# Optimization experiments

Measured on AMD Instinct MI355X. Metric: run time of the kernel, lower is better.

Reference implementation:

```python
import jax, jax.numpy as jnp
import numpy as np

EPS = 1e-5

def setup_inputs() -> dict:
    key = jax.random.key(0)
    kx, kq, kp = jax.random.split(key, 3)
    B, T, d = 4, 4096, 512
    x = jax.random.normal(kx, (B, T, d), dtype=jnp.float32)
    mask = jnp.tril(jnp.ones((T, T), dtype=jnp.int32))  # causal 0/1 mask
    gamma = jnp.ones((d,), dtype=jnp.float32)
    beta = jnp.zeros((d,), dtype=jnp.float32)
    Wqkv = jax.random.normal(kq, (d, 3 * d), dtype=jnp.float32) / np.sqrt(d)
    Wproj = jax.random.normal(kp, (d, d), dtype=jnp.float32) / np.sqrt(d)
    return {"x": x, "mask": mask, "gamma": gamma, "beta": beta, "Wqkv": Wqkv, "Wproj": Wproj}

def reference(x, mask, gamma, beta, Wqkv, Wproj):
    B, T, C = x.shape
    # LayerNorm over last dim
    mu = jnp.mean(x, axis=-1, keepdims=True)
    var = jnp.mean(jnp.square(x - mu), axis=-1, keepdims=True)
    xn = (x - mu) * jax.lax.rsqrt(var + EPS) * gamma + beta
    # QKV projection (no bias)
    qkv = xn @ Wqkv  # [B,T,3C]
    q, k, v = jnp.split(qkv, 3, axis=-1)
    scale = 1.0 / np.sqrt(C)
    dist = jnp.einsum('btc,bsc->bts', q, k) * scale  # [B,T,T]
    dist = jnp.where(mask[:T, :T] == 0, -jnp.inf, dist)
    attn = jax.nn.softmax(dist, axis=-1)
    out = jnp.einsum('bts,bsc->btc', attn, v)
    return out @ Wproj
```

## Files before the change

kernel.cpp:

```cpp
#include <hip/hip_runtime.h>

typedef short bf16x8 __attribute__((ext_vector_type(8)));
typedef float f32x4 __attribute__((ext_vector_type(4)));

#define AS1 __attribute__((address_space(1)))
#define AS3 __attribute__((address_space(3)))

__device__ __forceinline__ void async16(const void* g, void* l) {
    __builtin_amdgcn_global_load_lds((AS1 unsigned*)(unsigned long long)g,
                                     (AS3 unsigned*)l, 16, 0, 0);
}

__device__ __forceinline__ unsigned short f2bf(float f) {
    unsigned u = __builtin_bit_cast(unsigned, f);
    u += 0x7fffu + ((u >> 16) & 1u);
    return (unsigned short)(u >> 16);
}
__device__ __forceinline__ float bf2f(unsigned short s) {
    unsigned u = ((unsigned)s) << 16;
    return __builtin_bit_cast(float, u);
}

__global__ __launch_bounds__(256) void ln_bf16_kernel(
    const float* __restrict__ x, const float* __restrict__ gamma,
    const float* __restrict__ beta, unsigned short* __restrict__ xn, int nrows)
{
    int row = blockIdx.x * 4 + (threadIdx.x >> 6);
    int lane = threadIdx.x & 63;
    if (row >= nrows) return;
    const float4* xr = (const float4*)(x + (size_t)row * 512);
    float4 a = xr[lane], b = xr[lane + 64];
    float s = a.x + a.y + a.z + a.w + b.x + b.y + b.z + b.w;
    #pragma unroll
    for (int m = 1; m < 64; m <<= 1) s += __shfl_xor(s, m);
    float mu = s * (1.0f / 512.0f);
    float dx[8] = {a.x - mu, a.y - mu, a.z - mu, a.w - mu,
                   b.x - mu, b.y - mu, b.z - mu, b.w - mu};
    float ss = 0.f;
    #pragma unroll
    for (int i = 0; i < 8; ++i) ss += dx[i] * dx[i];
    #pragma unroll
    for (int m = 1; m < 64; m <<= 1) ss += __shfl_xor(ss, m);
    float rstd = rsqrtf(ss * (1.0f / 512.0f) + 1e-5f);
    const float4* gp = (const float4*)gamma;
    const float4* bp = (const float4*)beta;
    float4 g0 = gp[lane], g1 = gp[lane + 64], b0 = bp[lane], b1 = bp[lane + 64];
    float y[8];
    y[0] = dx[0] * rstd * g0.x + b0.x; y[1] = dx[1] * rstd * g0.y + b0.y;
    y[2] = dx[2] * rstd * g0.z + b0.z; y[3] = dx[3] * rstd * g0.w + b0.w;
    y[4] = dx[4] * rstd * g1.x + b1.x; y[5] = dx[5] * rstd * g1.y + b1.y;
    y[6] = dx[6] * rstd * g1.z + b1.z; y[7] = dx[7] * rstd * g1.w + b1.w;
    ushort4* orow = (ushort4*)(xn + (size_t)row * 512);
    orow[lane]      = make_ushort4(f2bf(y[0]), f2bf(y[1]), f2bf(y[2]), f2bf(y[3]));
    orow[lane + 64] = make_ushort4(f2bf(y[4]), f2bf(y[5]), f2bf(y[6]), f2bf(y[7]));
}

__global__ __launch_bounds__(256) void transpose_w2(
    const float* __restrict__ wqkv, const float* __restrict__ wproj,
    unsigned short* __restrict__ wqkvT, unsigned short* __restrict__ wprojT)
{
    __shared__ float tile[64][65];
    const int R = 512;
    int by = blockIdx.y;
    const float* in;
    unsigned short* outT;
    int Cd, c0;
    if (by < 24) { in = wqkv;  outT = wqkvT;  Cd = 1536; c0 = by * 64; }
    else         { in = wproj; outT = wprojT; Cd = 512;  c0 = (by - 24) * 64; }
    int r0 = blockIdx.x * 64;
    int lr = threadIdx.x >> 6, lc = threadIdx.x & 63;
    #pragma unroll
    for (int i = 0; i < 16; ++i) {
        int r = i * 4 + lr;
        tile[r][lc] = in[(size_t)(r0 + r) * Cd + c0 + lc];
    }
    __syncthreads();
    #pragma unroll
    for (int i = 0; i < 16; ++i) {
        int r = i * 4 + lr;
        outT[(size_t)(c0 + r) * R + r0 + lc] = f2bf(tile[lc][r]);
    }
}

__global__ __launch_bounds__(256) void gemm_qkv(
    const unsigned short* __restrict__ A, const unsigned short* __restrict__ Bt,
    unsigned short* __restrict__ qkOut, unsigned short* __restrict__ vtp)
{
    __shared__ unsigned short As[128 * 64];
    __shared__ unsigned short Bs[128 * 64];
    const int tid = threadIdx.x;
    const int w = tid >> 6, lane = tid & 63, quad = lane >> 4, l15 = lane & 15;
    const int wm = w >> 1, wn = w & 1;
    const size_t m0 = (size_t)blockIdx.x * 128, n0 = (size_t)blockIdx.y * 128;
    f32x4 zero = {0.f, 0.f, 0.f, 0.f};
    f32x4 acc[4][4];
    #pragma unroll
    for (int i = 0; i < 4; ++i)
        #pragma unroll
        for (int j = 0; j < 4; ++j) acc[i][j] = zero;

    for (int k0 = 0; k0 < 512; k0 += 64) {
        __syncthreads();
        #pragma unroll
        for (int r = 0; r < 4; ++r) {
            int s = r * 256 + w * 64 + lane;
            int row = s >> 3, x = s & 7, g = x ^ (row & 7);
            async16(A + (m0 + row) * 512 + k0 + g * 8,
                    (char*)As + (size_t)(r * 256 + w * 64) * 16);
        }
        #pragma unroll
        for (int r = 0; r < 4; ++r) {
            int s = r * 256 + w * 64 + lane;
            int row = s >> 3, x = s & 7, g = x ^ (row & 7);
            async16(Bt + (n0 + row) * 512 + k0 + g * 8,
                    (char*)Bs + (size_t)(r * 256 + w * 64) * 16);
        }
        __syncthreads();
        #pragma unroll
        for (int ks = 0; ks < 2; ++ks) {
            bf16x8 af[4], bf[4];
            int cc = ks * 4 + quad;
            #pragma unroll
            for (int mt = 0; mt < 4; ++mt) {
                int row = wm * 64 + mt * 16 + l15;
                int x = cc ^ (row & 7);
                af[mt] = *(const bf16x8*)(As + row * 64 + x * 8);
            }
            #pragma unroll
            for (int nt = 0; nt < 4; ++nt) {
                int row = wn * 64 + nt * 16 + l15;
                int x = cc ^ (row & 7);
                bf[nt] = *(const bf16x8*)(Bs + row * 64 + x * 8);
            }
            #pragma unroll
            for (int mt = 0; mt < 4; ++mt)
                #pragma unroll
                for (int nt = 0; nt < 4; ++nt)
                    acc[mt][nt] = __builtin_amdgcn_mfma_f32_16x16x32_bf16(
                        af[mt], bf[nt], acc[mt][nt], 0, 0, 0);
        }
    }
    if (n0 < 1024) {
        #pragma unroll
        for (int mt = 0; mt < 4; ++mt)
            #pragma unroll
            for (int nt = 0; nt < 4; ++nt)
                #pragma unroll
                for (int r = 0; r < 4; ++r) {
                    size_t grow = m0 + wm * 64 + mt * 16 + quad * 4 + r;
                    size_t gcol = n0 + wn * 64 + nt * 16 + l15;
                    qkOut[grow * 1024 + gcol] = f2bf(acc[mt][nt][r]);
                }
    } else {
        const int b = (int)(m0 >> 12);
        const int tb = (int)(m0 & 4095);
        #pragma unroll
        for (int mt = 0; mt < 4; ++mt)
            #pragma unroll
            for (int nt = 0; nt < 4; ++nt)
                #pragma unroll
                for (int r = 0; r < 4; ++r) {
                    int t = tb + wm * 64 + mt * 16 + quad * 4 + r;
                    int vcol = (int)(n0 - 1024) + wn * 64 + nt * 16 + l15;
                    int jt = t >> 5;
                    int x = (t >> 3) & 3;
                    vtp[(size_t)(b * 128 + jt) * 16384
                        + (size_t)(vcol * 4 + x) * 8 + (t & 7)] =
                        f2bf(acc[mt][nt][r]);
                }
    }
}

__global__ __launch_bounds__(256, 2) void attn_kernel(
    const unsigned short* __restrict__ qk,
    const unsigned short* __restrict__ vtp,
    unsigned short* __restrict__ ph0, unsigned short* __restrict__ ph1,
    float* __restrict__ lp)
{
    __shared__ unsigned short Ks[2][32 * 512];
    __shared__ unsigned short Ps[64 * 40];

    const int id = blockIdx.x;
    const int cu = id & 255, hi = id >> 8;
    const int b = cu & 3;
    const int q = hi ? (63 - (cu >> 2)) : (cu >> 2);
    const int h = hi;

    const int jt0 = h ? (q + 1) : 0;
    const int jtN = h ? (2 * q + 2) : (q + 1);

    const int tid = threadIdx.x, w = tid >> 6, lane = tid & 63;
    const int quad = lane >> 4, l15 = lane & 15;
    const float scale = 0.04419417382415922f;
    f32x4 zero = {0.f, 0.f, 0.f, 0.f};

    const unsigned short* kbase = qk + (size_t)(b * 4096) * 1024 + 512;
    const unsigned short* vbase = vtp + (size_t)(b * 128) * 16384;
    unsigned short* dst = h ? ph1 : ph0;

    const int gE = (lane & ~7) | ((lane ^ w) & 7);
    const int gO = (lane & ~7) | ((lane ^ (w + 4)) & 7);
    const size_t kOffE = (size_t)w * 1024 + (size_t)gE * 8;
    const size_t kOffO = (size_t)(w + 4) * 1024 + (size_t)gO * 8;
    const size_t vLane = (size_t)w * 4096 + (size_t)l15 * 32 + (size_t)quad * 8;

    bf16x8 qf[16];
    {
        const unsigned short* qb =
            qk + (size_t)(b * 4096 + q * 64 + w * 16 + l15) * 1024;
        #pragma unroll
        for (int ks = 0; ks < 16; ++ks)
            qf[ks] = *(const bf16x8*)(qb + ks * 32 + quad * 8);
    }
    f32x4 o[4][8];
    #pragma unroll
    for (int i = 0; i < 4; ++i)
        #pragma unroll
        for (int d = 0; d < 8; ++d) o[i][d] = zero;
    float li[4] = {0.f, 0.f, 0.f, 0.f};

    #define STAGE_K(BUF, T)                                                      \
    {                                                                            \
        const unsigned short* kg = kbase + (size_t)(T) * 32768;                  \
        _Pragma("unroll")                                                        \
        for (int rr = 0; rr < 4; ++rr) {                                         \
            async16(kg + (size_t)(2 * rr) * 4096 + kOffE,                        \
                    (char*)(&Ks[BUF][0]) + (size_t)((2 * rr) * 256 + w * 64) * 16);\
            async16(kg + (size_t)(2 * rr) * 4096 + kOffO,                        \
                    (char*)(&Ks[BUF][0]) + (size_t)((2 * rr + 1) * 256 + w * 64) * 16);\
        }                                                                        \
    }

    STAGE_K(0, jt0);
    __syncthreads();
    int cur = 0;

    for (int jt = jt0; jt < jtN; ++jt) {
        if (jt + 1 < jtN) STAGE_K(cur ^ 1, jt + 1);

        f32x4 sa[2];
        sa[0] = zero; sa[1] = zero;
        __builtin_amdgcn_s_setprio(1);
        #pragma unroll
        for (int ks = 0; ks < 16; ++ks) {
            int cc = ks * 4 + quad;
            #pragma unroll
            for (int nt = 0; nt < 2; ++nt) {
                int jr = nt * 16 + l15;
                int xg = (cc & ~7) | ((cc ^ jr) & 7);
                bf16x8 kf = *(const bf16x8*)(&Ks[cur][jr * 512 + xg * 8]);
                sa[nt] = __builtin_amdgcn_mfma_f32_16x16x32_bf16(
                    qf[ks], kf, sa[nt], 0, 0, 0);
            }
        }
        __builtin_amdgcn_s_setprio(0);
        const int trow = q * 64 + w * 16 + quad * 4;
        #pragma unroll
        for (int r = 0; r < 4; ++r) {
            #pragma unroll
            for (int nt = 0; nt < 2; ++nt) {
                int col = jt * 32 + nt * 16 + l15;
                float sv = sa[nt][r] * scale;
                float pv = __expf(fminf(sv, 60.f));
                if (col > trow + r) pv = 0.f;
                li[r] += pv;
                Ps[(w * 16 + quad * 4 + r) * 40 + nt * 16 + l15] = f2bf(pv);
            }
        }
        asm volatile("s_waitcnt lgkmcnt(0)" ::: "memory");
        __builtin_amdgcn_s_barrier();

        const unsigned short* vt = vbase + (size_t)jt * 16384 + vLane;
        bf16x8 vfr[8];
        #pragma unroll
        for (int i = 0; i < 8; ++i)
            vfr[i] = *(const bf16x8*)(vt + (size_t)i * 512);
        __builtin_amdgcn_s_setprio(1);
        #pragma unroll
        for (int qi = 0; qi < 4; ++qi) {
            bf16x8 pa = *(const bf16x8*)(Ps + (qi * 16 + l15) * 40 + quad * 8);
            #pragma unroll
            for (int i = 0; i < 8; ++i)
                o[qi][i] = __builtin_amdgcn_mfma_f32_16x16x32_bf16(
                    pa, vfr[i], o[qi][i], 0, 0, 0);
        }
        __builtin_amdgcn_s_setprio(0);
        __syncthreads();
        cur ^= 1;
    }
    #undef STAGE_K

    #pragma unroll
    for (int r = 0; r < 4; ++r) {
        float s = li[r];
        s += __shfl_xor(s, 1);
        s += __shfl_xor(s, 2);
        s += __shfl_xor(s, 4);
        s += __shfl_xor(s, 8);
        if (l15 == 0)
            lp[h * 16384 + b * 4096 + q * 64 + w * 16 + quad * 4 + r] = s;
    }
    unsigned short* ob = dst + (size_t)(b * 4096 + q * 64) * 512 + w * 128;
    #pragma unroll
    for (int qi = 0; qi < 4; ++qi)
        #pragma unroll
        for (int df = 0; df < 8; ++df)
            #pragma unroll
            for (int r = 0; r < 4; ++r)
                ob[(size_t)(qi * 16 + quad * 4 + r) * 512 + df * 16 + l15] =
                    f2bf(o[qi][df][r]);
}

__global__ __launch_bounds__(256) void gemm_proj(
    const unsigned short* __restrict__ ph0, const unsigned short* __restrict__ ph1,
    const float* __restrict__ lp, const unsigned short* __restrict__ Bt,
    float* __restrict__ out)
{
    __shared__ unsigned short As[128 * 64];
    __shared__ unsigned short Bs[128 * 64];
    const int tid = threadIdx.x;
    const int w = tid >> 6, lane = tid & 63, quad = lane >> 4, l15 = lane & 15;
    const int wm = w >> 1, wn = w & 1;
    const size_t m0 = (size_t)blockIdx.x * 128, n0 = (size_t)blockIdx.y * 128;
    f32x4 zero = {0.f, 0.f, 0.f, 0.f};
    f32x4 acc[4][4];
    #pragma unroll
    for (int i = 0; i < 4; ++i)
        #pragma unroll
        for (int j = 0; j < 4; ++j) acc[i][j] = zero;

    for (int k0 = 0; k0 < 512; k0 += 64) {
        __syncthreads();
        #pragma unroll
        for (int r = 0; r < 4; ++r) {
            int s = r * 256 + tid;
            int row = s >> 3, x = s & 7, g = x ^ (row & 7);
            size_t t = m0 + row;
            float inv = 1.0f / (lp[t] + lp[16384 + t]);
            bf16x8 a = *(const bf16x8*)(ph0 + t * 512 + k0 + g * 8);
            bf16x8 bb = *(const bf16x8*)(ph1 + t * 512 + k0 + g * 8);
            bf16x8 v;
            #pragma unroll
            for (int e = 0; e < 8; ++e)
                v[e] = (short)f2bf((bf2f((unsigned short)a[e])
                                  + bf2f((unsigned short)bb[e])) * inv);
            *(bf16x8*)(As + (size_t)s * 8) = v;
        }
        #pragma unroll
        for (int r = 0; r < 4; ++r) {
            int s = r * 256 + w * 64 + lane;
            int row = s >> 3, x = s & 7, g = x ^ (row & 7);
            async16(Bt + (n0 + row) * 512 + k0 + g * 8,
                    (char*)Bs + (size_t)(r * 256 + w * 64) * 16);
        }
        __syncthreads();
        #pragma unroll
        for (int ks = 0; ks < 2; ++ks) {
            bf16x8 af[4], bf[4];
            int cc = ks * 4 + quad;
            #pragma unroll
            for (int mt = 0; mt < 4; ++mt) {
                int row = wm * 64 + mt * 16 + l15;
                int x = cc ^ (row & 7);
                af[mt] = *(const bf16x8*)(As + row * 64 + x * 8);
            }
            #pragma unroll
            for (int nt = 0; nt < 4; ++nt) {
                int row = wn * 64 + nt * 16 + l15;
                int x = cc ^ (row & 7);
                bf[nt] = *(const bf16x8*)(Bs + row * 64 + x * 8);
            }
            #pragma unroll
            for (int mt = 0; mt < 4; ++mt)
                #pragma unroll
                for (int nt = 0; nt < 4; ++nt)
                    acc[mt][nt] = __builtin_amdgcn_mfma_f32_16x16x32_bf16(
                        af[mt], bf[nt], acc[mt][nt], 0, 0, 0);
        }
    }
    #pragma unroll
    for (int mt = 0; mt < 4; ++mt)
        #pragma unroll
        for (int nt = 0; nt < 4; ++nt)
            #pragma unroll
            for (int r = 0; r < 4; ++r) {
                size_t grow = m0 + wm * 64 + mt * 16 + quad * 4 + r;
                size_t gcol = n0 + wn * 64 + nt * 16 + l15;
                out[grow * 512 + gcol] = acc[mt][nt][r];
            }
}

extern "C" void kernel_launch(void* const* d_in, const int* in_sizes, int n_in,
                              void* d_out, int out_size, void* d_ws, size_t ws_size,
                              hipStream_t stream)
{
    const float* x     = (const float*)d_in[0];
    const float* gamma = (const float*)d_in[2];
    const float* beta  = (const float*)d_in[3];
    const float* Wqkv  = (const float*)d_in[4];
    const float* Wproj = (const float*)d_in[5];
    float* out = (float*)d_out;

    char* ws = (char*)d_ws;
    unsigned short* qk     = (unsigned short*)(ws);
    unsigned short* ph1    = (unsigned short*)(ws + 33554432);
    unsigned short* vtp    = (unsigned short*)(ws + 50331648);
    unsigned short* xn     = (unsigned short*)(ws + 67108864);
    unsigned short* wqkvT  = (unsigned short*)(ws + 83886080);
    unsigned short* wprojT = (unsigned short*)(ws + 85458944);
    unsigned short* ph0    = xn;
    float*          lp     = (float*)wqkvT;

    ln_bf16_kernel<<<4096, 256, 0, stream>>>(x, gamma, beta, xn, 16384);
    transpose_w2<<<dim3(8, 32), 256, 0, stream>>>(Wqkv, Wproj, wqkvT, wprojT);
    gemm_qkv<<<dim3(128, 12), 256, 0, stream>>>(xn, wqkvT, qk, vtp);
    attn_kernel<<<512, 256, 0, stream>>>(qk, vtp, ph0, ph1, lp);
    gemm_proj<<<dim3(128, 4), 256, 0, stream>>>(ph0, ph1, lp, wprojT, out);
}
```

Measured before the change: 341.9 us.

## Split causal KV range into quarters with float atomic accumulation of partial outputs

Each attention block now processes two query tiles (a and 63-a), each over one quarter of its causal KV range, instead of one tile over half the range. This evens out per-block work. Partial outputs and row sums are combined with float atomicAdd into fp32 buffers, which a new zero kernel clears first. The projection GEMM reads the fp32 accumulators directly. In exchange it adds an extra launch, fp32 atomic traffic (4 contributions per output element) and double-size intermediate reads, and summation order is no longer deterministic.

```diff
diff --git a/kernel.cpp b/kernel.cpp
--- a/kernel.cpp
+++ b/kernel.cpp
@@ -171,23 +171,31 @@
     }
 }
 
+__global__ __launch_bounds__(256) void zero_kernel(
+    float4* __restrict__ accLo, float4* __restrict__ accHi,
+    float4* __restrict__ lacc)
+{
+    const float4 z = {0.f, 0.f, 0.f, 0.f};
+    size_t stride = (size_t)gridDim.x * 256;
+    for (size_t i = blockIdx.x * 256 + threadIdx.x; i < 1048576; i += stride) {
+        accLo[i] = z;
+        accHi[i] = z;
+    }
+    for (size_t i = blockIdx.x * 256 + threadIdx.x; i < 4096; i += stride)
+        lacc[i] = z;
+}
+
 __global__ __launch_bounds__(256, 2) void attn_kernel(
     const unsigned short* __restrict__ qk,
     const unsigned short* __restrict__ vtp,
-    unsigned short* __restrict__ ph0, unsigned short* __restrict__ ph1,
-    float* __restrict__ lp)
+    float* __restrict__ accLo, float* __restrict__ accHi,
+    float* __restrict__ lacc)
 {
     __shared__ unsigned short Ks[2][32 * 512];
     __shared__ unsigned short Ps[64 * 40];
 
-    const int id = blockIdx.x;
-    const int cu = id & 255, hi = id >> 8;
-    const int b = cu & 3;
-    const int q = hi ? (63 - (cu >> 2)) : (cu >> 2);
-    const int h = hi;
-
-    const int jt0 = h ? (q + 1) : 0;
-    const int jtN = h ? (2 * q + 2) : (q + 1);
+    const int i = blockIdx.x;
+    const int a = i & 63, b = (i >> 6) & 3, j2 = i >> 8;
 
     const int tid = threadIdx.x, w = tid >> 6, lane = tid & 63;
     const int quad = lane >> 4, l15 = lane & 15;
@@ -196,28 +204,13 @@
 
     const unsigned short* kbase = qk + (size_t)(b * 4096) * 1024 + 512;
     const unsigned short* vbase = vtp + (size_t)(b * 128) * 16384;
-    unsigned short* dst = h ? ph1 : ph0;
+    float* accB = (b & 2) ? accHi : accLo;
 
     const int gE = (lane & ~7) | ((lane ^ w) & 7);
     const int gO = (lane & ~7) | ((lane ^ (w + 4)) & 7);
     const size_t kOffE = (size_t)w * 1024 + (size_t)gE * 8;
     const size_t kOffO = (size_t)(w + 4) * 1024 + (size_t)gO * 8;
     const size_t vLane = (size_t)w * 4096 + (size_t)l15 * 32 + (size_t)quad * 8;
-
-    bf16x8 qf[16];
-    {
-        const unsigned short* qb =
-            qk + (size_t)(b * 4096 + q * 64 + w * 16 + l15) * 1024;
-        #pragma unroll
-        for (int ks = 0; ks < 16; ++ks)
-            qf[ks] = *(const bf16x8*)(qb + ks * 32 + quad * 8);
-    }
-    f32x4 o[4][8];
-    #pragma unroll
-    for (int i = 0; i < 4; ++i)
-        #pragma unroll
-        for (int d = 0; d < 8; ++d) o[i][d] = zero;
-    float li[4] = {0.f, 0.f, 0.f, 0.f};
 
     #define STAGE_K(BUF, T)                                                      \
     {                                                                            \
@@ -231,89 +224,115 @@
         }                                                                        \
     }
 
-    STAGE_K(0, jt0);
-    __syncthreads();
-    int cur = 0;
-
-    for (int jt = jt0; jt < jtN; ++jt) {
-        if (jt + 1 < jtN) STAGE_K(cur ^ 1, jt + 1);
-
-        f32x4 sa[2];
-        sa[0] = zero; sa[1] = zero;
-        __builtin_amdgcn_s_setprio(1);
-        #pragma unroll
-        for (int ks = 0; ks < 16; ++ks) {
-            int cc = ks * 4 + quad;
-            #pragma unroll
-            for (int nt = 0; nt < 2; ++nt) {
-                int jr = nt * 16 + l15;
-                int xg = (cc & ~7) | ((cc ^ jr) & 7);
-                bf16x8 kf = *(const bf16x8*)(&Ks[cur][jr * 512 + xg * 8]);
-                sa[nt] = __builtin_amdgcn_mfma_f32_16x16x32_bf16(
-                    qf[ks], kf, sa[nt], 0, 0, 0);
-            }
-        }
-        __builtin_amdgcn_s_setprio(0);
-        const int trow = q * 64 + w * 16 + quad * 4;
+    #pragma unroll 1
+    for (int s = 0; s < 2; ++s) {
+        const int q = s ? (63 - a) : a;
+        const int j = s ? (j2 + 2) : j2;
+        const int T2 = 2 * q + 2;
+        const int t0 = (j * T2) >> 2;
+        const int t1 = ((j + 1) * T2) >> 2;
+        if (t0 >= t1) continue;
+
+        bf16x8 qf[16];
+        {
+            const unsigned short* qb =
+                qk + (size_t)(b * 4096 + q * 64 + w * 16 + l15) * 1024;
+            #pragma unroll
+            for (int ks = 0; ks < 16; ++ks)
+                qf[ks] = *(const bf16x8*)(qb + ks * 32 + quad * 8);
+        }
+        f32x4 o[4][8];
+        #pragma unroll
+        for (int ii = 0; ii < 4; ++ii)
+            #pragma unroll
+            for (int d = 0; d < 8; ++d) o[ii][d] = zero;
+        float li[4] = {0.f, 0.f, 0.f, 0.f};
+
+        STAGE_K(0, t0);
+        __syncthreads();
+        int cur = 0;
+
+        #pragma unroll 1
+        for (int jt = t0; jt < t1; ++jt) {
+            if (jt + 1 < t1) STAGE_K(cur ^ 1, jt + 1);
+
+            f32x4 sa[2];
+            sa[0] = zero; sa[1] = zero;
+            __builtin_amdgcn_s_setprio(1);
+            #pragma unroll
+            for (int ks = 0; ks < 16; ++ks) {
+                int cc = ks * 4 + quad;
+                #pragma unroll
+                for (int nt = 0; nt < 2; ++nt) {
+                    int jr = nt * 16 + l15;
+                    int xg = (cc & ~7) | ((cc ^ jr) & 7);
+                    bf16x8 kf = *(const bf16x8*)(&Ks[cur][jr * 512 + xg * 8]);
+                    sa[nt] = __builtin_amdgcn_mfma_f32_16x16x32_bf16(
+                        qf[ks], kf, sa[nt], 0, 0, 0);
+                }
+            }
+            __builtin_amdgcn_s_setprio(0);
+            const int trow = q * 64 + w * 16 + quad * 4;
+            #pragma unroll
+            for (int r = 0; r < 4; ++r) {
+                #pragma unroll
+                for (int nt = 0; nt < 2; ++nt) {
+                    int col = jt * 32 + nt * 16 + l15;
+                    float sv = sa[nt][r] * scale;
+                    float pv = __expf(fminf(sv, 60.f));
+                    if (col > trow + r) pv = 0.f;
+                    li[r] += pv;
+                    Ps[(w * 16 + quad * 4 + r) * 40 + nt * 16 + l15] = f2bf(pv);
+                }
+            }
+            asm volatile("s_waitcnt lgkmcnt(0)" ::: "memory");
+            __builtin_amdgcn_s_barrier();
+
+            const unsigned short* vt = vbase + (size_t)jt * 16384 + vLane;
+            bf16x8 vfr[8];
+            #pragma unroll
+            for (int ii = 0; ii < 8; ++ii)
+                vfr[ii] = *(const bf16x8*)(vt + (size_t)ii * 512);
+            __builtin_amdgcn_s_setprio(1);
+            #pragma unroll
+            for (int qi = 0; qi < 4; ++qi) {
+                bf16x8 pa = *(const bf16x8*)(Ps + (qi * 16 + l15) * 40 + quad * 8);
+                #pragma unroll
+                for (int ii = 0; ii < 8; ++ii)
+                    o[qi][ii] = __builtin_amdgcn_mfma_f32_16x16x32_bf16(
+                        pa, vfr[ii], o[qi][ii], 0, 0, 0);
+            }
+            __builtin_amdgcn_s_setprio(0);
+            __syncthreads();
+            cur ^= 1;
+        }
+
         #pragma unroll
         for (int r = 0; r < 4; ++r) {
-            #pragma unroll
-            for (int nt = 0; nt < 2; ++nt) {
-                int col = jt * 32 + nt * 16 + l15;
-                float sv = sa[nt][r] * scale;
-                float pv = __expf(fminf(sv, 60.f));
-                if (col > trow + r) pv = 0.f;
-                li[r] += pv;
-                Ps[(w * 16 + quad * 4 + r) * 40 + nt * 16 + l15] = f2bf(pv);
-            }
-        }
-        asm volatile("s_waitcnt lgkmcnt(0)" ::: "memory");
-        __builtin_amdgcn_s_barrier();
-
-        const unsigned short* vt = vbase + (size_t)jt * 16384 + vLane;
-        bf16x8 vfr[8];
-        #pragma unroll
-        for (int i = 0; i < 8; ++i)
-            vfr[i] = *(const bf16x8*)(vt + (size_t)i * 512);
-        __builtin_amdgcn_s_setprio(1);
-        #pragma unroll
-        for (int qi = 0; qi < 4; ++qi) {
-            bf16x8 pa = *(const bf16x8*)(Ps + (qi * 16 + l15) * 40 + quad * 8);
-            #pragma unroll
-            for (int i = 0; i < 8; ++i)
-                o[qi][i] = __builtin_amdgcn_mfma_f32_16x16x32_bf16(
-                    pa, vfr[i], o[qi][i], 0, 0, 0);
-        }
-        __builtin_amdgcn_s_setprio(0);
-        __syncthreads();
-        cur ^= 1;
+            float t = li[r];
+            t += __shfl_xor(t, 1);
+            t += __shfl_xor(t, 2);
+            t += __shfl_xor(t, 4);
+            t += __shfl_xor(t, 8);
+            if (l15 == 0)
+                atomicAdd(&lacc[b * 4096 + q * 64 + w * 16 + quad * 4 + r], t);
+        }
+        float* ab = accB + (size_t)((b & 1) * 4096 + q * 64) * 512 + w * 128;
+        #pragma unroll
+        for (int qi = 0; qi < 4; ++qi)
+            #pragma unroll
+            for (int df = 0; df < 8; ++df)
+                #pragma unroll
+                for (int r = 0; r < 4; ++r)
+                    atomicAdd(&ab[(size_t)(qi * 16 + quad * 4 + r) * 512
+                                  + df * 16 + l15], o[qi][df][r]);
     }
     #undef STAGE_K
-
-    #pragma unroll
-    for (int r = 0; r < 4; ++r) {
-        float s = li[r];
-        s += __shfl_xor(s, 1);
-        s += __shfl_xor(s, 2);
-        s += __shfl_xor(s, 4);
-        s += __shfl_xor(s, 8);
-        if (l15 == 0)
-            lp[h * 16384 + b * 4096 + q * 64 + w * 16 + quad * 4 + r] = s;
-    }
-    unsigned short* ob = dst + (size_t)(b * 4096 + q * 64) * 512 + w * 128;
-    #pragma unroll
-    for (int qi = 0; qi < 4; ++qi)
-        #pragma unroll
-        for (int df = 0; df < 8; ++df)
-            #pragma unroll
-            for (int r = 0; r < 4; ++r)
-                ob[(size_t)(qi * 16 + quad * 4 + r) * 512 + df * 16 + l15] =
-                    f2bf(o[qi][df][r]);
 }
 
 __global__ __launch_bounds__(256) void gemm_proj(
-    const unsigned short* __restrict__ ph0, const unsigned short* __restrict__ ph1,
-    const float* __restrict__ lp, const unsigned short* __restrict__ Bt,
+    const float* __restrict__ accLo, const float* __restrict__ accHi,
+    const float* __restrict__ lacc, const unsigned short* __restrict__ Bt,
     float* __restrict__ out)
 {
     __shared__ unsigned short As[128 * 64];
@@ -322,6 +341,7 @@
     const int w = tid >> 6, lane = tid & 63, quad = lane >> 4, l15 = lane & 15;
     const int wm = w >> 1, wn = w & 1;
     const size_t m0 = (size_t)blockIdx.x * 128, n0 = (size_t)blockIdx.y * 128;
+    const float* accB = (m0 < 8192) ? accLo : accHi;
     f32x4 zero = {0.f, 0.f, 0.f, 0.f};
     f32x4 acc[4][4];
     #pragma unroll
@@ -336,14 +356,15 @@
             int s = r * 256 + tid;
             int row = s >> 3, x = s & 7, g = x ^ (row & 7);
             size_t t = m0 + row;
-            float inv = 1.0f / (lp[t] + lp[16384 + t]);
-            bf16x8 a = *(const bf16x8*)(ph0 + t * 512 + k0 + g * 8);
-            bf16x8 bb = *(const bf16x8*)(ph1 + t * 512 + k0 + g * 8);
+            float inv = 1.0f / lacc[t];
+            const float* src = accB + ((size_t)(t & 8191)) * 512 + k0 + g * 8;
+            float4 fa = *(const float4*)(src);
+            float4 fb = *(const float4*)(src + 4);
             bf16x8 v;
-            #pragma unroll
-            for (int e = 0; e < 8; ++e)
-                v[e] = (short)f2bf((bf2f((unsigned short)a[e])
-                                  + bf2f((unsigned short)bb[e])) * inv);
+            v[0] = (short)f2bf(fa.x * inv); v[1] = (short)f2bf(fa.y * inv);
+            v[2] = (short)f2bf(fa.z * inv); v[3] = (short)f2bf(fa.w * inv);
+            v[4] = (short)f2bf(fb.x * inv); v[5] = (short)f2bf(fb.y * inv);
+            v[6] = (short)f2bf(fb.z * inv); v[7] = (short)f2bf(fb.w * inv);
             *(bf16x8*)(As + (size_t)s * 8) = v;
         }
         #pragma unroll
@@ -403,17 +424,19 @@
 
     char* ws = (char*)d_ws;
     unsigned short* qk     = (unsigned short*)(ws);
-    unsigned short* ph1    = (unsigned short*)(ws + 33554432);
+    float*          accLo  = (float*)(ws + 33554432);
     unsigned short* vtp    = (unsigned short*)(ws + 50331648);
     unsigned short* xn     = (unsigned short*)(ws + 67108864);
     unsigned short* wqkvT  = (unsigned short*)(ws + 83886080);
     unsigned short* wprojT = (unsigned short*)(ws + 85458944);
-    unsigned short* ph0    = xn;
-    float*          lp     = (float*)wqkvT;
+    float*          accHi  = (float*)xn;
+    float*          lacc   = (float*)wqkvT;
 
     ln_bf16_kernel<<<4096, 256, 0, stream>>>(x, gamma, beta, xn, 16384);
     transpose_w2<<<dim3(8, 32), 256, 0, stream>>>(Wqkv, Wproj, wqkvT, wprojT);
     gemm_qkv<<<dim3(128, 12), 256, 0, stream>>>(xn, wqkvT, qk, vtp);
-    attn_kernel<<<512, 256, 0, stream>>>(qk, vtp, ph0, ph1, lp);
-    gemm_proj<<<dim3(128, 4), 256, 0, stream>>>(ph0, ph1, lp, wprojT, out);
-}
+    zero_kernel<<<1024, 256, 0, stream>>>((float4*)accLo, (float4*)accHi,
+                                          (float4*)lacc);
+    attn_kernel<<<512, 256, 0, stream>>>(qk, vtp, accLo, accHi, lacc);
+    gemm_proj<<<dim3(128, 4), 256, 0, stream>>>(accLo, accHi, lacc, wprojT, out);
+}
```

New measurement: 477.8 us. 1.4x slower.
